# Kernel tuning notes

Hardware: AMD Instinct MI355X
Metric: run time of the kernel (lower is better)

The kernel has to match this reference:

```python
import jax, jax.numpy as jnp
import numpy as np

WINDOW_SIZE = 11
SIGMA = 1.5
C1 = 0.01 ** 2
C2 = 0.03 ** 2
LAMBDA_DSSIM = 0.2


def _gaussian_window(channel):
    x = jnp.arange(WINDOW_SIZE, dtype=jnp.float32)
    g = jnp.exp(-((x - WINDOW_SIZE // 2) ** 2) / (2.0 * SIGMA ** 2))
    g = g / g.sum()
    w2d = jnp.outer(g, g)  # [ws, ws]
    # depthwise kernel: [O=C, I=1, ws, ws]
    return jnp.broadcast_to(w2d[None, None], (channel, 1, WINDOW_SIZE, WINDOW_SIZE))


def _dwconv(x, window, channel):
    # x: [1, C, H, W]; same padding ws//2, depthwise (groups=C)
    pad = WINDOW_SIZE // 2
    return jax.lax.conv_general_dilated(
        x, window,
        window_strides=(1, 1),
        padding=((pad, pad), (pad, pad)),
        dimension_numbers=("NCHW", "OIHW", "NCHW"),
        feature_group_count=channel,
    )


def _ssim_mean(img1, img2):
    # img1, img2: [C, H, W]
    channel = img1.shape[0]
    window = _gaussian_window(channel).astype(img1.dtype)
    a = img1[None]  # [1, C, H, W]
    b = img2[None]

    mu1 = _dwconv(a, window, channel)
    mu2 = _dwconv(b, window, channel)
    mu1_sq = mu1 * mu1
    mu2_sq = mu2 * mu2
    mu1_mu2 = mu1 * mu2
    sigma1_sq = _dwconv(a * a, window, channel) - mu1_sq
    sigma2_sq = _dwconv(b * b, window, channel) - mu2_sq
    sigma12 = _dwconv(a * b, window, channel) - mu1_mu2

    ssim_map = ((2 * mu1_mu2 + C1) * (2 * sigma12 + C2)) / (
        (mu1_sq + mu2_sq + C1) * (sigma1_sq + sigma2_sq + C2))
    return ssim_map.mean()


def setup_inputs() -> dict:
    key = jax.random.key(0)
    k1, k2 = jax.random.split(key)
    shape = (3, 2160, 3840)
    pred = jax.random.uniform(k1, shape, dtype=jnp.float32)
    target = jax.random.uniform(k2, shape, dtype=jnp.float32)
    return {"pred": pred, "target": target}


def reference(pred, target):
    l1 = jnp.abs(pred - target).mean()
    ssim_val = _ssim_mean(pred, target)
    return (1.0 - LAMBDA_DSSIM) * l1 + LAMBDA_DSSIM * (1.0 - ssim_val)
```

## Files before the change

kernel.cpp:

```cpp
#include <hip/hip_runtime.h>
#include <math.h>

#define WSZ 11
#define PAD 5
#define TX 32
#define TY 24
#define NY 6
#define IY (TY + 2*PAD)
#define RX 4
#define NTASK0 (IY * 8)
#define NTASK1 (TY * 8)
#define SEG (RX + 2*PAD)
#define RY 3
#define SA 33

typedef float v2f __attribute__((ext_vector_type(2)));

struct W11 { float w[WSZ]; };

__global__ __launch_bounds__(256, 4) void ssim_l1_kernel(
    const float* __restrict__ pred, const float* __restrict__ targ,
    W11 wt, float2* __restrict__ partials)
{
    constexpr int H = 2160, W = 3840;
    __shared__ float4 sHA[IY][SA];

    const int c    = blockIdx.z;
    const int gx0  = blockIdx.x * TX;
    const int base = blockIdx.y * (TY * NY);
    const size_t plane = (size_t)H * W;
    const float* p = pred + (size_t)c * plane;
    const float* t = targ + (size_t)c * plane;

    const int tid = threadIdx.x;
    v2f loss_acc = {0.f, 0.f};
    const float C1v = 0.0001f, C2v = 0.0009f;

    const int oxB  = tid & 31;
    const int oy0B = (tid >> 5) * RY;
    const bool xfast = (blockIdx.x >= 1) && (blockIdx.x <= (W / TX) - 2);

    for (int s = 0; s < NY; ++s) {
        if (s > 0) {
            for (int i = tid; i < 2 * PAD * TX; i += 256) {
                const int dr = i >> 5, cc = i & 31;
                sHA[dr][cc] = sHA[dr + TY][cc];
            }
            __syncthreads();
        }

        const int ntask  = (s == 0) ? NTASK0 : NTASK1;
        const int rowoff = (s == 0) ? 0 : 2 * PAD;
        const int gyA    = base + TY * s - PAD;
        for (int task = tid; task < ntask; task += 256) {
            const int r  = task >> 3;
            const int cx = task & 7;
            const int rr = rowoff + r;
            const int gy = gyA + rr;
            const int gxs = gx0 + cx * RX - PAD;
            const bool rowok   = (gy >= 0) && (gy < H);
            const bool own_row = (gy >= base) && (gy < base + TY * NY);

            float4 P[5], T[5];
            if (rowok && xfast) {
                const float4* p4 = (const float4*)(p + (size_t)gy * W + (gxs - 3));
                const float4* t4 = (const float4*)(t + (size_t)gy * W + (gxs - 3));
                #pragma unroll
                for (int i = 0; i < 5; ++i) { P[i] = p4[i]; T[i] = t4[i]; }
            } else if (rowok) {
                const size_t rowoff2 = (size_t)gy * W;
                #pragma unroll
                for (int i = 0; i < 5; ++i) {
                    float pe[4], te[4];
                    #pragma unroll
                    for (int q = 0; q < 4; ++q) {
                        int gx = gxs - 3 + 4 * i + q;
                        bool ok = (gx >= 0) && (gx < W);
                        pe[q] = ok ? p[rowoff2 + gx] : 0.f;
                        te[q] = ok ? t[rowoff2 + gx] : 0.f;
                    }
                    P[i] = make_float4(pe[0], pe[1], pe[2], pe[3]);
                    T[i] = make_float4(te[0], te[1], te[2], te[3]);
                }
            } else {
                #pragma unroll
                for (int i = 0; i < 5; ++i) {
                    P[i] = make_float4(0.f, 0.f, 0.f, 0.f);
                    T[i] = make_float4(0.f, 0.f, 0.f, 0.f);
                }
            }

            v2f h_sd[RX], h_qq[RX];
            #pragma unroll
            for (int j = 0; j < RX; ++j) {
                h_sd[j] = (v2f){0.f, 0.f};
                h_qq[j] = (v2f){0.f, 0.f};
            }
            #pragma unroll
            for (int e = 0; e < SEG; ++e) {
                const int ii = (e + 3) >> 2, qq = (e + 3) & 3;
                const float pe = (qq == 0) ? P[ii].x : (qq == 1) ? P[ii].y
                                : (qq == 2) ? P[ii].z : P[ii].w;
                const float te = (qq == 0) ? T[ii].x : (qq == 1) ? T[ii].y
                                : (qq == 2) ? T[ii].z : T[ii].w;
                v2f vsd; vsd.x = pe + te; vsd.y = pe - te;
                const v2f vsq = vsd * vsd;
                #pragma unroll
                for (int j = 0; j < RX; ++j) {
                    const int k = e - j;
                    if (k >= 0 && k < WSZ) {
                        const float wv = wt.w[k];
                        h_sd[j] += wv * vsd;
                        h_qq[j] += wv * vsq;
                    }
                }
                if (e >= PAD && e < PAD + RX && own_row)
                    loss_acc.y += fabsf(vsd.y);
            }
            const int xb = cx * RX;
            #pragma unroll
            for (int j = 0; j < RX; ++j)
                sHA[rr][xb + j] = make_float4(h_sd[j].x, h_sd[j].y,
                                              h_qq[j].x, h_qq[j].y);
        }
        __syncthreads();

        {
            v2f mu[RY], qq[RY];
            #pragma unroll
            for (int j = 0; j < RY; ++j) {
                mu[j] = (v2f){0.f, 0.f};
                qq[j] = (v2f){0.f, 0.f};
            }
            #pragma unroll
            for (int k = 0; k < RY + 2 * PAD; ++k) {
                const float4 f = sHA[oy0B + k][oxB];
                v2f fsd; fsd.x = f.x; fsd.y = f.y;
                v2f fsq; fsq.x = f.z; fsq.y = f.w;
                #pragma unroll
                for (int j = 0; j < RY; ++j) {
                    const int kk = k - j;
                    if (kk >= 0 && kk < WSZ) {
                        const float wv = wt.w[kk];
                        mu[j] += wv * fsd;
                        qq[j] += wv * fsq;
                    }
                }
            }
            #pragma unroll
            for (int j = 0; j < RY; ++j) {
                const v2f musq = mu[j] * mu[j];
                const v2f rr2  = qq[j] - musq;
                const float a  = 0.5f * (musq.x - musq.y) + C1v;
                const float b  = 0.5f * (rr2.x - rr2.y) + C2v;
                const float cden = 0.5f * (musq.x + musq.y) + C1v;
                const float dden = 0.5f * (rr2.x + rr2.y) + C2v;
                loss_acc.x += (a * b) * __builtin_amdgcn_rcpf(cden * dden);
            }
        }
        __syncthreads();
    }

    #pragma unroll
    for (int off = 32; off > 0; off >>= 1) {
        loss_acc.x += __shfl_down(loss_acc.x, off, 64);
        loss_acc.y += __shfl_down(loss_acc.y, off, 64);
    }
    __shared__ float red[2][4];
    const int lane = tid & 63;
    const int wid  = tid >> 6;
    if (lane == 0) { red[0][wid] = loss_acc.x; red[1][wid] = loss_acc.y; }
    __syncthreads();
    if (tid == 0) {
        const float sv = red[0][0] + red[0][1] + red[0][2] + red[0][3];
        const float lv = red[1][0] + red[1][1] + red[1][2] + red[1][3];
        const int bid = (blockIdx.z * gridDim.y + blockIdx.y) * gridDim.x + blockIdx.x;
        partials[bid] = make_float2(sv, lv);
    }
}

__global__ __launch_bounds__(256) void finalize_kernel(
    const float2* __restrict__ partials, int n,
    float* __restrict__ out, double invN)
{
    const int tid = threadIdx.x;
    double s = 0.0, l = 0.0;
    for (int i = tid; i < n; i += 256) {
        float2 v = partials[i];
        s += (double)v.x;
        l += (double)v.y;
    }
    #pragma unroll
    for (int off = 32; off > 0; off >>= 1) {
        s += __shfl_down(s, off, 64);
        l += __shfl_down(l, off, 64);
    }
    __shared__ double rs[4], rl[4];
    const int lane = tid & 63, wid = tid >> 6;
    if (lane == 0) { rs[wid] = s; rl[wid] = l; }
    __syncthreads();
    if (tid == 0) {
        const double st = rs[0] + rs[1] + rs[2] + rs[3];
        const double lt = rl[0] + rl[1] + rl[2] + rl[3];
        out[0] = (float)(0.8 * lt * invN + 0.2 * (1.0 - st * invN));
    }
}

extern "C" void kernel_launch(void* const* d_in, const int* in_sizes, int n_in,
                              void* d_out, int out_size, void* d_ws, size_t ws_size,
                              hipStream_t stream)
{
    const float* pred = (const float*)d_in[0];
    const float* targ = (const float*)d_in[1];
    float* out = (float*)d_out;
    float2* partials = (float2*)d_ws;

    const int C = 3, H = 2160, W = 3840;

    W11 wt;
    double g[WSZ], sg = 0.0;
    for (int i = 0; i < WSZ; ++i) {
        double d = (double)i - (WSZ / 2);
        g[i] = exp(-(d * d) / (2.0 * 1.5 * 1.5));
        sg += g[i];
    }
    for (int i = 0; i < WSZ; ++i) wt.w[i] = (float)(g[i] / sg);

    dim3 grid(W / TX, H / (TY * NY), C);
    ssim_l1_kernel<<<grid, 256, 0, stream>>>(pred, targ, wt, partials);

    const int nblocks = (W / TX) * (H / (TY * NY)) * C;
    double invN = 1.0 / ((double)C * (double)H * (double)W);
    finalize_kernel<<<1, 256, 0, stream>>>(partials, nblocks, out, invN);
}
```

Before: 246.8 us.

## Recast separable Gaussian convolutions as fp16 MFMA matmuls with hi/lo weight split

Replaces the scalar FMA-based horizontal and vertical 11-tap convolutions with 16x16x32 f16 MFMA instructions. Banded weight matrices are split into hi and lo fp16 parts to recover precision. Blocks shrink to a single 64-thread wavefront over a 16-wide by 144-row strip, with swizzled fp16-packed LDS staging between the two passes. This aims to offload the conv arithmetic to matrix cores, but rounding inputs and intermediates to fp16 risks accuracy, and the small blocks re-read more halo data from memory.

```diff
diff --git a/kernel.cpp b/kernel.cpp
--- a/kernel.cpp
+++ b/kernel.cpp
@@ -2,180 +2,188 @@
 #include <math.h>
 
 #define WSZ 11
-#define PAD 5
-#define TX 32
-#define TY 24
-#define NY 6
-#define IY (TY + 2*PAD)
-#define RX 4
-#define NTASK0 (IY * 8)
-#define NTASK1 (TY * 8)
-#define SEG (RX + 2*PAD)
-#define RY 3
-#define SA 33
-
-typedef float v2f __attribute__((ext_vector_type(2)));
+#define RB 144
+
+typedef float f32x4 __attribute__((ext_vector_type(4)));
+typedef unsigned int u32;
+typedef u32 u32x4 __attribute__((ext_vector_type(4)));
+typedef _Float16 f16;
+typedef _Float16 f16x2v __attribute__((ext_vector_type(2)));
+typedef _Float16 f16x8 __attribute__((ext_vector_type(8)));
 
 struct W11 { float w[WSZ]; };
 
-__global__ __launch_bounds__(256, 4) void ssim_l1_kernel(
+__device__ inline u32 packpair(float a, float b) {
+    f16x2v v; v[0] = (f16)a; v[1] = (f16)b;
+    return __builtin_bit_cast(u32, v);
+}
+
+__global__ __launch_bounds__(64, 4) void ssim_l1_kernel(
     const float* __restrict__ pred, const float* __restrict__ targ,
     W11 wt, float2* __restrict__ partials)
 {
     constexpr int H = 2160, W = 3840;
-    __shared__ float4 sHA[IY][SA];
-
-    const int c    = blockIdx.z;
-    const int gx0  = blockIdx.x * TX;
-    const int base = blockIdx.y * (TY * NY);
+    __shared__ u32x4 Hbuf4[4][16][4];
+
+    const int bx = blockIdx.x, c = blockIdx.z;
+    const int x0   = bx * 16;
+    const int base = blockIdx.y * RB;
     const size_t plane = (size_t)H * W;
     const float* p = pred + (size_t)c * plane;
     const float* t = targ + (size_t)c * plane;
 
-    const int tid = threadIdx.x;
-    v2f loss_acc = {0.f, 0.f};
+    const int l   = threadIdx.x;
+    const int xl  = l & 15;
+    const int g   = l >> 4;
+    const int swz = (xl & 3) << 2;
+    u32* Hw = (u32*)Hbuf4;
+
+    float lssim = 0.f, ll1 = 0.f;
     const float C1v = 0.0001f, C2v = 0.0009f;
-
-    const int oxB  = tid & 31;
-    const int oy0B = (tid >> 5) * RY;
-    const bool xfast = (blockIdx.x >= 1) && (blockIdx.x <= (W / TX) - 2);
-
-    for (int s = 0; s < NY; ++s) {
-        if (s > 0) {
-            for (int i = tid; i < 2 * PAD * TX; i += 256) {
-                const int dr = i >> 5, cc = i & 31;
-                sHA[dr][cc] = sHA[dr + TY][cc];
+    const bool xfast = (bx >= 1) && (bx <= (W / 16) - 3);
+    const f32x4 z4 = {0.f, 0.f, 0.f, 0.f};
+
+    f16x8 Whi, Wlo;
+    #pragma unroll
+    for (int j = 0; j < 8; ++j) {
+        const int idx = 8 * g + j - xl;
+        float wv = 0.f;
+        #pragma unroll
+        for (int tI = 0; tI < WSZ; ++tI) wv = (idx == tI) ? wt.w[tI] : wv;
+        const f16 hi = (f16)wv;
+        Whi[j] = hi;
+        Wlo[j] = (f16)(wv - (float)hi);
+    }
+
+    #pragma unroll
+    for (int wq = 13; wq <= 15; ++wq)
+        Hw[(g * 16 + xl) * 16 + (wq ^ swz)] = 0u;
+    __syncthreads();
+
+    f32x4 hS, hD, hQs, hQd;
+
+    auto phaseL = [&](const int gy0, const int mlo, const int mhi) {
+        const int gy = gy0 + xl;
+        const bool rowok = (gy >= 0) && (gy < H);
+        float pe[12], te[12];
+        if (rowok && xfast) {
+            const f32x4* p4 = (const f32x4*)(p + (size_t)gy * W + (x0 + 8 * g - 8));
+            const f32x4* t4 = (const f32x4*)(t + (size_t)gy * W + (x0 + 8 * g - 8));
+            #pragma unroll
+            for (int i = 0; i < 3; ++i) {
+                const f32x4 a = p4[i], b = t4[i];
+                #pragma unroll
+                for (int q = 0; q < 4; ++q) { pe[4*i+q] = a[q]; te[4*i+q] = b[q]; }
             }
-            __syncthreads();
-        }
-
-        const int ntask  = (s == 0) ? NTASK0 : NTASK1;
-        const int rowoff = (s == 0) ? 0 : 2 * PAD;
-        const int gyA    = base + TY * s - PAD;
-        for (int task = tid; task < ntask; task += 256) {
-            const int r  = task >> 3;
-            const int cx = task & 7;
-            const int rr = rowoff + r;
-            const int gy = gyA + rr;
-            const int gxs = gx0 + cx * RX - PAD;
-            const bool rowok   = (gy >= 0) && (gy < H);
-            const bool own_row = (gy >= base) && (gy < base + TY * NY);
-
-            float4 P[5], T[5];
-            if (rowok && xfast) {
-                const float4* p4 = (const float4*)(p + (size_t)gy * W + (gxs - 3));
-                const float4* t4 = (const float4*)(t + (size_t)gy * W + (gxs - 3));
-                #pragma unroll
-                for (int i = 0; i < 5; ++i) { P[i] = p4[i]; T[i] = t4[i]; }
-            } else if (rowok) {
-                const size_t rowoff2 = (size_t)gy * W;
-                #pragma unroll
-                for (int i = 0; i < 5; ++i) {
-                    float pe[4], te[4];
-                    #pragma unroll
-                    for (int q = 0; q < 4; ++q) {
-                        int gx = gxs - 3 + 4 * i + q;
-                        bool ok = (gx >= 0) && (gx < W);
-                        pe[q] = ok ? p[rowoff2 + gx] : 0.f;
-                        te[q] = ok ? t[rowoff2 + gx] : 0.f;
-                    }
-                    P[i] = make_float4(pe[0], pe[1], pe[2], pe[3]);
-                    T[i] = make_float4(te[0], te[1], te[2], te[3]);
-                }
-            } else {
-                #pragma unroll
-                for (int i = 0; i < 5; ++i) {
-                    P[i] = make_float4(0.f, 0.f, 0.f, 0.f);
-                    T[i] = make_float4(0.f, 0.f, 0.f, 0.f);
-                }
+        } else if (rowok) {
+            const size_t ro = (size_t)gy * W;
+            #pragma unroll
+            for (int e = 0; e < 12; ++e) {
+                const int gx = x0 + 8 * g - 8 + e;
+                const bool ok = (gx >= 0) && (gx < W);
+                pe[e] = ok ? p[ro + gx] : 0.f;
+                te[e] = ok ? t[ro + gx] : 0.f;
             }
-
-            v2f h_sd[RX], h_qq[RX];
-            #pragma unroll
-            for (int j = 0; j < RX; ++j) {
-                h_sd[j] = (v2f){0.f, 0.f};
-                h_qq[j] = (v2f){0.f, 0.f};
-            }
-            #pragma unroll
-            for (int e = 0; e < SEG; ++e) {
-                const int ii = (e + 3) >> 2, qq = (e + 3) & 3;
-                const float pe = (qq == 0) ? P[ii].x : (qq == 1) ? P[ii].y
-                                : (qq == 2) ? P[ii].z : P[ii].w;
-                const float te = (qq == 0) ? T[ii].x : (qq == 1) ? T[ii].y
-                                : (qq == 2) ? T[ii].z : T[ii].w;
-                v2f vsd; vsd.x = pe + te; vsd.y = pe - te;
-                const v2f vsq = vsd * vsd;
-                #pragma unroll
-                for (int j = 0; j < RX; ++j) {
-                    const int k = e - j;
-                    if (k >= 0 && k < WSZ) {
-                        const float wv = wt.w[k];
-                        h_sd[j] += wv * vsd;
-                        h_qq[j] += wv * vsq;
-                    }
-                }
-                if (e >= PAD && e < PAD + RX && own_row)
-                    loss_acc.y += fabsf(vsd.y);
-            }
-            const int xb = cx * RX;
-            #pragma unroll
-            for (int j = 0; j < RX; ++j)
-                sHA[rr][xb + j] = make_float4(h_sd[j].x, h_sd[j].y,
-                                              h_qq[j].x, h_qq[j].y);
-        }
+        } else {
+            #pragma unroll
+            for (int e = 0; e < 12; ++e) { pe[e] = 0.f; te[e] = 0.f; }
+        }
+        float sv[8], dv[8];
+        #pragma unroll
+        for (int j = 0; j < 8; ++j) {
+            sv[j] = pe[j + 3] + te[j + 3];
+            dv[j] = pe[j + 3] - te[j + 3];
+        }
+        {
+            float s1 = 0.f, s2 = 0.f;
+            #pragma unroll
+            for (int j = 0; j < 5; ++j) s1 += fabsf(dv[j]);
+            #pragma unroll
+            for (int j = 5; j < 8; ++j) s2 += fabsf(dv[j]);
+            const float own = (g == 0) ? s2 : (g == 1) ? (s1 + s2)
+                            : (g == 2) ? s1 : 0.f;
+            if (xl >= mlo && xl <= mhi) ll1 += own;
+        }
+        f16x8 fS, fD, fQs, fQd;
+        #pragma unroll
+        for (int j = 0; j < 8; ++j) {
+            fS[j]  = (f16)sv[j];
+            fD[j]  = (f16)dv[j];
+            fQs[j] = (f16)(sv[j] * sv[j]);
+            fQd[j] = (f16)(dv[j] * dv[j]);
+        }
+        hS  = __builtin_amdgcn_mfma_f32_16x16x32_f16(fS,  Whi, z4, 0, 0, 0);
+        hS  = __builtin_amdgcn_mfma_f32_16x16x32_f16(fS,  Wlo, hS, 0, 0, 0);
+        hD  = __builtin_amdgcn_mfma_f32_16x16x32_f16(fD,  Whi, z4, 0, 0, 0);
+        hD  = __builtin_amdgcn_mfma_f32_16x16x32_f16(fD,  Wlo, hD, 0, 0, 0);
+        hQs = __builtin_amdgcn_mfma_f32_16x16x32_f16(fQs, Whi, z4, 0, 0, 0);
+        hQs = __builtin_amdgcn_mfma_f32_16x16x32_f16(fQs, Wlo, hQs, 0, 0, 0);
+        hQd = __builtin_amdgcn_mfma_f32_16x16x32_f16(fQd, Whi, z4, 0, 0, 0);
+        hQd = __builtin_amdgcn_mfma_f32_16x16x32_f16(fQd, Wlo, hQd, 0, 0, 0);
+    };
+
+    auto hwrite = [&](const int a0) {
+        const int w0 = ((a0 >> 1) + 2 * g) & 15;
+        const int w1 = (w0 + 1) & 15;
+        Hw[(0 * 16 + xl) * 16 + (w0 ^ swz)] = packpair(hS[0],  hS[1]);
+        Hw[(0 * 16 + xl) * 16 + (w1 ^ swz)] = packpair(hS[2],  hS[3]);
+        Hw[(1 * 16 + xl) * 16 + (w0 ^ swz)] = packpair(hD[0],  hD[1]);
+        Hw[(1 * 16 + xl) * 16 + (w1 ^ swz)] = packpair(hD[2],  hD[3]);
+        Hw[(2 * 16 + xl) * 16 + (w0 ^ swz)] = packpair(hQs[0], hQs[1]);
+        Hw[(2 * 16 + xl) * 16 + (w1 ^ swz)] = packpair(hQs[2], hQs[3]);
+        Hw[(3 * 16 + xl) * 16 + (w0 ^ swz)] = packpair(hQd[0], hQd[1]);
+        Hw[(3 * 16 + xl) * 16 + (w1 ^ swz)] = packpair(hQd[2], hQd[3]);
+    };
+
+    auto vphase = [&](const int s) {
+        const int q = (((2 * s) + g) & 3) ^ (xl & 3);
+        f16x8 hb;
+        f32x4 aS, aD, aQs, aQd;
+        hb = __builtin_bit_cast(f16x8, Hbuf4[0][xl][q]);
+        aS = __builtin_amdgcn_mfma_f32_16x16x32_f16(Whi, hb, z4, 0, 0, 0);
+        aS = __builtin_amdgcn_mfma_f32_16x16x32_f16(Wlo, hb, aS, 0, 0, 0);
+        hb = __builtin_bit_cast(f16x8, Hbuf4[1][xl][q]);
+        aD = __builtin_amdgcn_mfma_f32_16x16x32_f16(Whi, hb, z4, 0, 0, 0);
+        aD = __builtin_amdgcn_mfma_f32_16x16x32_f16(Wlo, hb, aD, 0, 0, 0);
+        hb = __builtin_bit_cast(f16x8, Hbuf4[2][xl][q]);
+        aQs = __builtin_amdgcn_mfma_f32_16x16x32_f16(Whi, hb, z4, 0, 0, 0);
+        aQs = __builtin_amdgcn_mfma_f32_16x16x32_f16(Wlo, hb, aQs, 0, 0, 0);
+        hb = __builtin_bit_cast(f16x8, Hbuf4[3][xl][q]);
+        aQd = __builtin_amdgcn_mfma_f32_16x16x32_f16(Whi, hb, z4, 0, 0, 0);
+        aQd = __builtin_amdgcn_mfma_f32_16x16x32_f16(Wlo, hb, aQd, 0, 0, 0);
+        #pragma unroll
+        for (int r = 0; r < 4; ++r) {
+            const float S = aS[r], D = aD[r];
+            const float S2 = S * S, D2 = D * D;
+            const float rs = aQs[r] - S2, rd = aQd[r] - D2;
+            const float a  = 0.5f * (S2 - D2) + C1v;
+            const float b  = 0.5f * (rs - rd) + C2v;
+            const float cd = 0.5f * (S2 + D2) + C1v;
+            const float dd = 0.5f * (rs + rd) + C2v;
+            lssim += (a * b) * __builtin_amdgcn_rcpf(cd * dd);
+        }
+    };
+
+    phaseL(base - 5, 5, 15);  hwrite(0);
+    phaseL(base + 5, 6, 15);  hwrite(10);
+    __syncthreads();
+    vphase(0);
+    for (int s = 1; s <= 8; ++s) {
+        phaseL(base + 16 * s + 5, 0, (s == 8) ? 10 : 15);
         __syncthreads();
-
-        {
-            v2f mu[RY], qq[RY];
-            #pragma unroll
-            for (int j = 0; j < RY; ++j) {
-                mu[j] = (v2f){0.f, 0.f};
-                qq[j] = (v2f){0.f, 0.f};
-            }
-            #pragma unroll
-            for (int k = 0; k < RY + 2 * PAD; ++k) {
-                const float4 f = sHA[oy0B + k][oxB];
-                v2f fsd; fsd.x = f.x; fsd.y = f.y;
-                v2f fsq; fsq.x = f.z; fsq.y = f.w;
-                #pragma unroll
-                for (int j = 0; j < RY; ++j) {
-                    const int kk = k - j;
-                    if (kk >= 0 && kk < WSZ) {
-                        const float wv = wt.w[kk];
-                        mu[j] += wv * fsd;
-                        qq[j] += wv * fsq;
-                    }
-                }
-            }
-            #pragma unroll
-            for (int j = 0; j < RY; ++j) {
-                const v2f musq = mu[j] * mu[j];
-                const v2f rr2  = qq[j] - musq;
-                const float a  = 0.5f * (musq.x - musq.y) + C1v;
-                const float b  = 0.5f * (rr2.x - rr2.y) + C2v;
-                const float cden = 0.5f * (musq.x + musq.y) + C1v;
-                const float dden = 0.5f * (rr2.x + rr2.y) + C2v;
-                loss_acc.x += (a * b) * __builtin_amdgcn_rcpf(cden * dden);
-            }
-        }
+        hwrite((16 * s + 10) & 31);
         __syncthreads();
+        vphase(s);
     }
 
     #pragma unroll
     for (int off = 32; off > 0; off >>= 1) {
-        loss_acc.x += __shfl_down(loss_acc.x, off, 64);
-        loss_acc.y += __shfl_down(loss_acc.y, off, 64);
-    }
-    __shared__ float red[2][4];
-    const int lane = tid & 63;
-    const int wid  = tid >> 6;
-    if (lane == 0) { red[0][wid] = loss_acc.x; red[1][wid] = loss_acc.y; }
-    __syncthreads();
-    if (tid == 0) {
-        const float sv = red[0][0] + red[0][1] + red[0][2] + red[0][3];
-        const float lv = red[1][0] + red[1][1] + red[1][2] + red[1][3];
+        lssim += __shfl_down(lssim, off, 64);
+        ll1   += __shfl_down(ll1,   off, 64);
+    }
+    if (l == 0) {
         const int bid = (blockIdx.z * gridDim.y + blockIdx.y) * gridDim.x + blockIdx.x;
-        partials[bid] = make_float2(sv, lv);
+        partials[bid] = make_float2(lssim, ll1);
     }
 }
 
@@ -226,10 +234,10 @@
     }
     for (int i = 0; i < WSZ; ++i) wt.w[i] = (float)(g[i] / sg);
 
-    dim3 grid(W / TX, H / (TY * NY), C);
-    ssim_l1_kernel<<<grid, 256, 0, stream>>>(pred, targ, wt, partials);
-
-    const int nblocks = (W / TX) * (H / (TY * NY)) * C;
+    dim3 grid(W / 16, H / RB, C);
+    ssim_l1_kernel<<<grid, 64, 0, stream>>>(pred, targ, wt, partials);
+
+    const int nblocks = (W / 16) * (H / RB) * C;
     double invN = 1.0 / ((double)C * (double)H * (double)W);
     finalize_kernel<<<1, 256, 0, stream>>>(partials, nblocks, out, invN);
 }
```

Result: slower. 299.0 us (+21.1%).
